# Kernel optimization log

Measured on AMD Instinct MI355X. Metric: run time of the kernel, lower is better.

The kernel has to match this reference:

```python
import jax, jax.numpy as jnp
import numpy as np

EPS = 1e-5


def _grid_edges(H, W):
    # radius_graph on the HxW integer grid with r=1.0, loop=False -> 4-neighbors,
    # then GCNConv's gcn_norm adds self-loops; we append them here once.
    idx = np.arange(H * W).reshape(H, W)
    r_s, r_d = idx[:, :-1].ravel(), idx[:, 1:].ravel()
    d_s, d_d = idx[:-1, :].ravel(), idx[1:, :].ravel()
    loop = np.arange(H * W)
    src = np.concatenate([r_s, r_d, d_s, d_d, loop])
    dst = np.concatenate([r_d, r_s, d_d, d_s, loop])
    return jnp.asarray(src, jnp.int32), jnp.asarray(dst, jnp.int32)


def _gcn_conv(x, W, b, src, dst, deg, dinv):
    # GCNConv(aggr='mean'): xw = x @ W; message = dinv[src]*dinv[dst] * xw[src];
    # mean-aggregate over incoming edges (incl. self-loop); add bias.
    xw = x @ W  # [B, N, Cout]
    w = (dinv[src] * dinv[dst])[None, :, None]
    agg = jnp.zeros((x.shape[0], x.shape[1], W.shape[1]), xw.dtype).at[:, dst].add(xw[:, src] * w)
    return agg / deg[None, :, None] + b


def _bn(x, gamma, beta):
    # BatchNorm2d, training-mode batch statistics (torch default), biased variance
    mu = x.mean(axis=(0, 2, 3), keepdims=True)
    var = ((x - mu) ** 2).mean(axis=(0, 2, 3), keepdims=True)
    return (x - mu) * jax.lax.rsqrt(var + EPS) * gamma[None, :, None, None] + beta[None, :, None, None]


def setup_inputs() -> dict:
    key = jax.random.key(0)
    ks = jax.random.split(key, 5)
    B, H, W, Cin, Cout = 8, 64, 64, 512, 512
    s = 0.02
    return {
        'x': jax.random.normal(ks[0], (B, H * W, Cin), jnp.float32),
        'H': H, 'W': W,
        'w_res': jax.random.normal(ks[1], (Cin, Cout), jnp.float32) * s,
        'w_pre': jax.random.normal(ks[2], (Cin, Cout), jnp.float32) * s,
        'b_pre': jnp.zeros((Cout,), jnp.float32),
        'w_g1': jax.random.normal(ks[3], (Cout, Cout), jnp.float32) * s,
        'b_g1': jnp.zeros((Cout,), jnp.float32),
        'w_g2': jax.random.normal(ks[4], (Cout, Cout), jnp.float32) * s,
        'b_g2': jnp.zeros((Cout,), jnp.float32),
        'g1': jnp.ones((Cout,), jnp.float32), 'beta1': jnp.zeros((Cout,), jnp.float32),
        'g2': jnp.ones((Cout,), jnp.float32), 'beta2': jnp.zeros((Cout,), jnp.float32),
    }


def reference(x, H, W, w_res, w_pre, b_pre, w_g1, b_g1, w_g2, b_g2, g1, beta1, g2, beta2):
    B, N, Cin = x.shape
    src, dst = _grid_edges(H, W)
    deg = jnp.zeros((N,), x.dtype).at[dst].add(1.0)  # in-degree incl. self-loops
    dinv = jax.lax.rsqrt(deg)
    # 1x1 convs on tokens == per-node matmuls
    residual = jnp.einsum('bnc,cd->bnd', x, w_res)
    xr = jnp.einsum('bnc,cd->bnd', x, w_pre) + b_pre
    h = jax.nn.relu(_gcn_conv(xr, w_g1, b_g1, src, dst, deg, dinv))
    h = jax.nn.relu(_gcn_conv(h, w_g2, b_g2, src, dst, deg, dinv))
    pooled = h.mean(axis=1)  # global_mean_pool -> [B, Cout]
    xg = _bn(pooled[:, :, None, None], g1, beta1)  # [B, Cout, 1, 1]
    res_img = residual.transpose(0, 2, 1).reshape(B, -1, H, W)
    return _bn(res_img + xg, g2, beta2)  # [B, Cout, H, W]
```

## Files before the change

kernel.cpp:

```cpp
#include <hip/hip_runtime.h>
#include <hip/hip_bf16.h>

using bf16 = __hip_bfloat16;
typedef __attribute__((ext_vector_type(8))) __bf16 bf16x8;
typedef __attribute__((ext_vector_type(4))) float f32x4;

__device__ __forceinline__ float bf2f(bf16 v) { return __bfloat162float(v); }
__device__ __forceinline__ bf16 f2bf(float f) { return __float2bfloat16(f); }

union bfu8 { bf16x8 v; bf16 h[8]; int4 i; };

__device__ __forceinline__ bool probeF32(const unsigned* probe) {
    return probe != nullptr && probe[0] == 0x3F800000u;
}
__device__ __forceinline__ float ldIn(const void* p, int i, bool f32) {
    return f32 ? ((const float*)p)[i] : bf2f(((const bf16*)p)[i]);
}

#define BATCH 8
#define GRID 64
#define NNODE 4096
#define CDIM 512
#define MROWS 32768
#define EPSBN 1e-5f

#define BM 128
#define BN 128
#define BK 32

__device__ __forceinline__ void gload16(bf16* lds, const bf16* g) {
    __builtin_amdgcn_global_load_lds(
        (const __attribute__((address_space(1))) unsigned int*)g,
        (__attribute__((address_space(3))) unsigned int*)lds, 16, 0, 0);
}

#define PIN() __builtin_amdgcn_sched_barrier(0)

__global__ __launch_bounds__(256) void gemm_lds(const bf16* __restrict__ A,
                                                const bf16* __restrict__ BT,
                                                bf16* __restrict__ C0,
                                                bf16* __restrict__ C1,
                                                const void* __restrict__ bias,
                                                const unsigned* __restrict__ probe,
                                                int K)
{
    __shared__ __align__(16) bf16 lA[2][BM * BK];
    __shared__ __align__(16) bf16 lB[2][BN * BK];

    const bool pf32 = probeF32(probe);
    const int tid  = threadIdx.x;
    const int bm = blockIdx.x, bn = blockIdx.y;
    const int wave = tid >> 6, lane = tid & 63;
    const int wr = (wave >> 1) * 64, wc = (wave & 1) * 64;
    const int lrow = lane & 15, quad = lane >> 4;

    f32x4 acc[4][4] = {};

    const bf16* Abase = A  + (size_t)bm * BM * K;
    const bf16* Bbase = BT + (size_t)bn * BN * K;

    const int srow = wave * 32 + (lane >> 2);
    const int scol = (lane & 3) * 8;
    const bf16* gA0 = Abase + (size_t)srow * K + scol;
    const bf16* gA1 = Abase + (size_t)(srow + 16) * K + scol;
    const bf16* gB0 = Bbase + (size_t)srow * K + scol;
    const bf16* gB1 = Bbase + (size_t)(srow + 16) * K + scol;
    bf16* laBase = &lA[0][0];
    bf16* lbBase = &lB[0][0];
    const int wofs = wave * 1024;

#define STAGE(BUF, TILE) do {                                              \
        const size_t koff_ = (size_t)(TILE) * BK;                          \
        gload16(laBase + (BUF) * (BM * BK) + wofs,       gA0 + koff_);     \
        gload16(laBase + (BUF) * (BM * BK) + wofs + 512, gA1 + koff_);     \
        gload16(lbBase + (BUF) * (BN * BK) + wofs,       gB0 + koff_);     \
        gload16(lbBase + (BUF) * (BN * BK) + wofs + 512, gB1 + koff_);     \
    } while (0)

#define COMPUTE(BUF) do {                                                  \
        const bf16* pA_ = laBase + (BUF) * (BM * BK);                      \
        const bf16* pB_ = lbBase + (BUF) * (BN * BK);                      \
        bf16x8 af[4], bv[4];                                               \
        _Pragma("unroll")                                                  \
        for (int i = 0; i < 4; ++i)                                        \
            af[i] = *(const bf16x8*)(pA_ + (wr + i * 16 + lrow) * BK + quad * 8); \
        _Pragma("unroll")                                                  \
        for (int j = 0; j < 4; ++j)                                        \
            bv[j] = *(const bf16x8*)(pB_ + (wc + j * 16 + lrow) * BK + quad * 8); \
        _Pragma("unroll")                                                  \
        for (int i = 0; i < 4; ++i)                                        \
            _Pragma("unroll")                                              \
            for (int j = 0; j < 4; ++j)                                    \
                acc[i][j] = __builtin_amdgcn_mfma_f32_16x16x32_bf16(af[i], bv[j], acc[i][j], 0, 0, 0); \
    } while (0)

    const int NT = K / BK;

    STAGE(0, 0);
    int t = 0;
    for (; t + 3 < NT; t += 2) {
        STAGE(1, t + 1);
        asm volatile("s_waitcnt vmcnt(4)" ::: "memory");
        __builtin_amdgcn_s_barrier(); PIN();
        COMPUTE(0);
        PIN(); __builtin_amdgcn_s_barrier(); PIN();

        STAGE(0, t + 2);
        asm volatile("s_waitcnt vmcnt(4)" ::: "memory");
        __builtin_amdgcn_s_barrier(); PIN();
        COMPUTE(1);
        PIN(); __builtin_amdgcn_s_barrier(); PIN();
    }
    STAGE(1, t + 1);
    asm volatile("s_waitcnt vmcnt(4)" ::: "memory");
    __builtin_amdgcn_s_barrier(); PIN();
    COMPUTE(0);
    PIN(); __builtin_amdgcn_s_barrier(); PIN();
    asm volatile("s_waitcnt vmcnt(0)" ::: "memory");
    __builtin_amdgcn_s_barrier(); PIN();
    COMPUTE(1);

#undef STAGE
#undef COMPUTE

    #pragma unroll
    for (int i = 0; i < 4; ++i) {
        const int mbase = bm * BM + wr + i * 16 + quad * 4;
        #pragma unroll
        for (int j = 0; j < 4; ++j) {
            int n = bn * BN + wc + j * 16 + lrow;
            bf16* Cd = C0;
            float bvv = 0.0f;
            if (C1 != nullptr && n >= CDIM) { Cd = C1; n -= CDIM; }
            else if (bias != nullptr)       { bvv = ldIn(bias, n, pf32); }
            #pragma unroll
            for (int rr = 0; rr < 4; ++rr)
                Cd[(size_t)(mbase + rr) * CDIM + n] = f2bf(acc[i][j][rr] + bvv);
        }
    }
}

__global__ __launch_bounds__(256) void convertX(const void* __restrict__ x,
                                                bf16* __restrict__ xb,
                                                const unsigned* __restrict__ probe)
{
    const bool f32 = probeF32(probe);
    const size_t i = ((size_t)blockIdx.x * 256 + threadIdx.x) * 8;
    if (f32) {
        const float4 u0 = *(const float4*)((const float*)x + i);
        const float4 u1 = *(const float4*)((const float*)x + i + 4);
        bf16 t[8] = { f2bf(u0.x), f2bf(u0.y), f2bf(u0.z), f2bf(u0.w),
                      f2bf(u1.x), f2bf(u1.y), f2bf(u1.z), f2bf(u1.w) };
        *(int4*)(xb + i) = *(const int4*)t;
    } else {
        *(int4*)(xb + i) = *(const int4*)((const bf16*)x + i);
    }
}

__global__ __launch_bounds__(256) void transpose512x4(const void* __restrict__ s0,
                                                      const void* __restrict__ s1,
                                                      const void* __restrict__ s2,
                                                      const void* __restrict__ s3,
                                                      bf16* __restrict__ dstBase,
                                                      const unsigned* __restrict__ probe)
{
    __shared__ float tile[64][65];
    const bool f32 = probeF32(probe);
    const int z = blockIdx.z;
    const void* src = (z == 0) ? s0 : (z == 1) ? s1 : (z == 2) ? s2 : s3;
    bf16* dst = dstBase + (size_t)z * 512 * 512;
    const int bx = blockIdx.x, by = blockIdx.y;
    const int t = threadIdx.x;
    const int col = t & 63, rbase = t >> 6;
    #pragma unroll 4
    for (int i = 0; i < 16; ++i) {
        int r = i * 4 + rbase;
        tile[r][col] = ldIn(src, (by * 64 + r) * 512 + bx * 64 + col, f32);
    }
    __syncthreads();
    #pragma unroll 4
    for (int i = 0; i < 16; ++i) {
        int r = i * 4 + rbase;
        dst[(size_t)(bx * 64 + r) * 512 + by * 64 + col] = f2bf(tile[col][r]);
    }
}

__device__ __forceinline__ float degOf(int y, int x) {
    return 1.0f + (y > 0) + (y < GRID - 1) + (x > 0) + (x < GRID - 1);
}

__global__ __launch_bounds__(256) void gcn_agg_v2(const bf16* __restrict__ T,
                                                  const void* __restrict__ bias,
                                                  const unsigned* __restrict__ probe,
                                                  bf16* __restrict__ H)
{
    const bool f32 = probeF32(probe);
    const int t = threadIdx.x;
    const int lane = t & 63, sub = t >> 6;
    const int n = blockIdx.x * 4 + sub;
    const int b = blockIdx.y;
    const int y = n >> 6, x = n & 63;
    const int cg = lane * 8;

    const float deg = degOf(y, x);
    const float dn  = rsqrtf(deg);
    const float inv = dn / deg;

    const bf16* cptr = T + ((size_t)b * NNODE + n) * CDIM + cg;

    bfu8 vc; vc.v = *(const bf16x8*)cptr;
    float s[8];
    #pragma unroll
    for (int j = 0; j < 8; ++j) s[j] = dn * bf2f(vc.h[j]);

    if (y > 0)        { float d = rsqrtf(degOf(y - 1, x)); bfu8 u; u.v = *(const bf16x8*)(cptr - 64 * CDIM);
                        #pragma unroll
                        for (int j = 0; j < 8; ++j) s[j] += d * bf2f(u.h[j]); }
    if (y < GRID - 1) { float d = rsqrtf(degOf(y + 1, x)); bfu8 u; u.v = *(const bf16x8*)(cptr + 64 * CDIM);
                        #pragma unroll
                        for (int j = 0; j < 8; ++j) s[j] += d * bf2f(u.h[j]); }
    if (x > 0)        { float d = rsqrtf(degOf(y, x - 1)); bfu8 u; u.v = *(const bf16x8*)(cptr - CDIM);
                        #pragma unroll
                        for (int j = 0; j < 8; ++j) s[j] += d * bf2f(u.h[j]); }
    if (x < GRID - 1) { float d = rsqrtf(degOf(y, x + 1)); bfu8 u; u.v = *(const bf16x8*)(cptr + CDIM);
                        #pragma unroll
                        for (int j = 0; j < 8; ++j) s[j] += d * bf2f(u.h[j]); }

    bfu8 o;
    #pragma unroll
    for (int j = 0; j < 8; ++j)
        o.h[j] = f2bf(fmaxf(s[j] * inv + ldIn(bias, cg + j, f32), 0.0f));
    *(int4*)(H + ((size_t)b * NNODE + n) * CDIM + cg) = o.i;
}

__global__ __launch_bounds__(256) void gcn_agg_pool_v3(const bf16* __restrict__ T,
                                                       const void* __restrict__ bias,
                                                       const unsigned* __restrict__ probe,
                                                       float* __restrict__ poolPart)
{
    const bool f32 = probeF32(probe);
    const int y = blockIdx.x;
    const int b = blockIdx.y;
    const int t = threadIdx.x;
    const int lane = t & 63, sub = t >> 6;
    const int cg = lane * 8;

    const bf16* base = T + (size_t)b * NNODE * CDIM;

    float biasv[8];
    #pragma unroll
    for (int j = 0; j < 8; ++j) biasv[j] = ldIn(bias, cg + j, f32);

    float acc[8] = {};

    for (int xi = 0; xi < 16; ++xi) {
        const int x = sub * 16 + xi;
        const int n = y * 64 + x;
        const float deg = degOf(y, x);
        const float dn  = rsqrtf(deg);
        const float inv = dn / deg;
        const bf16* cptr = base + (size_t)n * CDIM + cg;

        bfu8 vc; vc.v = *(const bf16x8*)cptr;
        float s[8];
        #pragma unroll
        for (int j = 0; j < 8; ++j) s[j] = dn * bf2f(vc.h[j]);

        if (y > 0)        { float d = rsqrtf(degOf(y - 1, x)); bfu8 u; u.v = *(const bf16x8*)(cptr - 64 * CDIM);
                            #pragma unroll
                            for (int j = 0; j < 8; ++j) s[j] += d * bf2f(u.h[j]); }
        if (y < GRID - 1) { float d = rsqrtf(degOf(y + 1, x)); bfu8 u; u.v = *(const bf16x8*)(cptr + 64 * CDIM);
                            #pragma unroll
                            for (int j = 0; j < 8; ++j) s[j] += d * bf2f(u.h[j]); }
        if (x > 0)        { float d = rsqrtf(degOf(y, x - 1)); bfu8 u; u.v = *(const bf16x8*)(cptr - CDIM);
                            #pragma unroll
                            for (int j = 0; j < 8; ++j) s[j] += d * bf2f(u.h[j]); }
        if (x < GRID - 1) { float d = rsqrtf(degOf(y, x + 1)); bfu8 u; u.v = *(const bf16x8*)(cptr + CDIM);
                            #pragma unroll
                            for (int j = 0; j < 8; ++j) s[j] += d * bf2f(u.h[j]); }

        #pragma unroll
        for (int j = 0; j < 8; ++j)
            acc[j] += fmaxf(s[j] * inv + biasv[j], 0.0f);
    }

    __shared__ float red[4][64][9];
    #pragma unroll
    for (int j = 0; j < 8; ++j) red[sub][lane][j] = acc[j];
    __syncthreads();
    if (sub == 0) {
        float* dst = poolPart + (size_t)(b * GRID + y) * CDIM + cg;
        #pragma unroll
        for (int j = 0; j < 8; ++j)
            dst[j] = red[0][lane][j] + red[1][lane][j] + red[2][lane][j] + red[3][lane][j];
    }
}

__global__ void bn1_kernel(const float* __restrict__ poolPart,
                           const void* __restrict__ g1, const void* __restrict__ beta1,
                           const unsigned* __restrict__ probe,
                           float* __restrict__ xg)
{
    const bool f32 = probeF32(probe);
    const int c = blockIdx.x * 256 + threadIdx.x;
    float p[BATCH];
    float mu = 0.0f;
    #pragma unroll
    for (int b = 0; b < BATCH; ++b) {
        float a0 = 0, a1 = 0, a2 = 0, a3 = 0;
        const float* src = poolPart + (size_t)b * GRID * CDIM + c;
        #pragma unroll 4
        for (int y = 0; y < GRID; y += 4) {
            a0 += src[(size_t)(y + 0) * CDIM];
            a1 += src[(size_t)(y + 1) * CDIM];
            a2 += src[(size_t)(y + 2) * CDIM];
            a3 += src[(size_t)(y + 3) * CDIM];
        }
        p[b] = (a0 + a1 + a2 + a3) * (1.0f / (float)NNODE);
        mu += p[b];
    }
    mu *= (1.0f / (float)BATCH);
    float var = 0.0f;
    #pragma unroll
    for (int b = 0; b < BATCH; ++b) { float d = p[b] - mu; var += d * d; }
    var *= (1.0f / (float)BATCH);
    const float rs = rsqrtf(var + EPSBN) * ldIn(g1, c, f32);
    const float bt = ldIn(beta1, c, f32);
    #pragma unroll
    for (int b = 0; b < BATCH; ++b)
        xg[b * CDIM + c] = (p[b] - mu) * rs + bt;
}

__global__ __launch_bounds__(256) void bn2_stats_part(const bf16* __restrict__ R,
                                                      const float* __restrict__ xg,
                                                      float* __restrict__ bn2Part)
{
    const int t = threadIdx.x;
    const int lane = t & 63, sub = t >> 6;
    const int cg = lane * 8;
    const int row0 = blockIdx.x * 128;
    const int b = row0 >> 12;

    float xgv[8];
    #pragma unroll
    for (int j = 0; j < 8; ++j) xgv[j] = xg[b * CDIM + cg + j];

    float s[8] = {}, q[8] = {};
    #pragma unroll
    for (int i0 = 0; i0 < 4; ++i0) {
        const bf16* base = R + (size_t)(row0 + i0 * 32 + sub * 8) * CDIM + cg;
        #pragma unroll
        for (int k = 0; k < 8; ++k) {
            bfu8 u; u.v = *(const bf16x8*)(base + (size_t)k * CDIM);
            #pragma unroll
            for (int j = 0; j < 8; ++j) {
                float v = bf2f(u.h[j]) + xgv[j];
                s[j] += v; q[j] += v * v;
            }
        }
    }

    __shared__ float redS[4][64][9], redQ[4][64][9];
    #pragma unroll
    for (int j = 0; j < 8; ++j) { redS[sub][lane][j] = s[j]; redQ[sub][lane][j] = q[j]; }
    __syncthreads();
    if (sub == 0) {
        float* dst = bn2Part + (size_t)blockIdx.x * 1024;
        #pragma unroll
        for (int j = 0; j < 8; ++j) {
            dst[cg + j]       = redS[0][lane][j] + redS[1][lane][j] + redS[2][lane][j] + redS[3][lane][j];
            dst[512 + cg + j] = redQ[0][lane][j] + redQ[1][lane][j] + redQ[2][lane][j] + redQ[3][lane][j];
        }
    }
}

__global__ void bn2_reduce(const float* __restrict__ bn2Part, float* __restrict__ sums)
{
    const int c = blockIdx.x * 256 + threadIdx.x;
    float a0 = 0, a1 = 0, a2 = 0, a3 = 0, a4 = 0, a5 = 0, a6 = 0, a7 = 0;
    #pragma unroll 4
    for (int blk = 0; blk < 256; blk += 8) {
        a0 += bn2Part[(size_t)(blk + 0) * 1024 + c];
        a1 += bn2Part[(size_t)(blk + 1) * 1024 + c];
        a2 += bn2Part[(size_t)(blk + 2) * 1024 + c];
        a3 += bn2Part[(size_t)(blk + 3) * 1024 + c];
        a4 += bn2Part[(size_t)(blk + 4) * 1024 + c];
        a5 += bn2Part[(size_t)(blk + 5) * 1024 + c];
        a6 += bn2Part[(size_t)(blk + 6) * 1024 + c];
        a7 += bn2Part[(size_t)(blk + 7) * 1024 + c];
    }
    sums[c] = ((a0 + a1) + (a2 + a3)) + ((a4 + a5) + (a6 + a7));
}

__global__ void bn2_final(const float* __restrict__ sums, const float* __restrict__ xg,
                          const void* __restrict__ g2, const void* __restrict__ beta2,
                          const unsigned* __restrict__ probe,
                          float* __restrict__ scale, float* __restrict__ tshift)
{
    const bool f32 = probeF32(probe);
    const int c = blockIdx.x * 256 + threadIdx.x;
    const float mu  = sums[c] * (1.0f / (float)MROWS);
    const float var = sums[512 + c] * (1.0f / (float)MROWS) - mu * mu;
    const float sc  = ldIn(g2, c, f32) * rsqrtf(var + EPSBN);
    scale[c] = sc;
    const float base = ldIn(beta2, c, f32) - mu * sc;
    #pragma unroll
    for (int b = 0; b < BATCH; ++b)
        tshift[b * CDIM + c] = xg[b * CDIM + c] * sc + base;
}

__global__ __launch_bounds__(256) void out_transpose(const bf16* __restrict__ R,
                                                     const float* __restrict__ scale,
                                                     const float* __restrict__ tshift,
                                                     const unsigned* __restrict__ probe,
                                                     void* __restrict__ outv)
{
    __shared__ float tile[64][65];
    const bool f32 = probeF32(probe);
    const int nt = blockIdx.x;
    const int ct = blockIdx.y;
    const int b  = blockIdx.z;
    const int t = threadIdx.x;
    const int c0 = ct * 64, n0 = nt * 64;

    const int rr  = t >> 3;
    const int cch = (t & 7) * 8;
    #pragma unroll
    for (int half = 0; half < 2; ++half) {
        int r = rr + half * 32;
        bfu8 u; u.v = *(const bf16x8*)(R + ((size_t)(b * NNODE + n0 + r)) * CDIM + c0 + cch);
        #pragma unroll
        for (int j = 0; j < 8; ++j) tile[r][cch + j] = bf2f(u.h[j]);
    }
    __syncthreads();

    const int col = t & 63, rbase = t >> 6;
    if (f32) {
        float* out = (float*)outv;
        #pragma unroll 4
        for (int i = 0; i < 16; ++i) {
            int cc = i * 4 + rbase;
            float sc  = scale[c0 + cc];
            float tsh = tshift[b * CDIM + c0 + cc];
            out[((size_t)(b * CDIM + c0 + cc)) * NNODE + n0 + col] = tile[col][cc] * sc + tsh;
        }
    } else {
        bf16* out = (bf16*)outv;
        #pragma unroll 4
        for (int i = 0; i < 16; ++i) {
            int cc = i * 4 + rbase;
            float sc  = scale[c0 + cc];
            float tsh = tshift[b * CDIM + c0 + cc];
            out[((size_t)(b * CDIM + c0 + cc)) * NNODE + n0 + col] = f2bf(tile[col][cc] * sc + tsh);
        }
    }
}

extern "C" void kernel_launch(void* const* d_in, const int* in_sizes, int n_in,
                              void* d_out, int out_size, void* d_ws, size_t ws_size,
                              hipStream_t stream)
{
    const void* x     = d_in[0];
    const void* w_res = d_in[3];
    const void* w_pre = d_in[4];
    const void* b_pre = d_in[5];
    const void* w_g1  = d_in[6];
    const void* b_g1  = d_in[7];
    const void* w_g2  = d_in[8];
    const void* b_g2  = d_in[9];
    const void* g1    = d_in[10];
    const void* beta1 = d_in[11];
    const void* g2    = d_in[12];
    const void* beta2 = d_in[13];
    const unsigned* probe = (const unsigned*)g1;

    char* ws = (char*)d_ws;
    constexpr size_t WSZ = (size_t)512 * 512 * 2;

    bf16* BTpre = (bf16*)(ws);
    bf16* BTg1  = (bf16*)(ws + 2 * WSZ);
    bf16* BTg2  = (bf16*)(ws + 3 * WSZ);
    char* smallb = ws + 4 * WSZ;
    float* sums   = (float*)(smallb);
    float* xg     = (float*)(smallb + 4096);
    float* scale  = (float*)(smallb + 4096 + 16384);
    float* tshift = (float*)(smallb + 4096 + 16384 + 2048);
    bf16* Rres = (bf16*)(smallb + 65536);

    char* dA = (char*)d_out;
    char* dB = (char*)d_out + (size_t)MROWS * CDIM * 2;

    bf16* XR = (bf16*)dA;
    bf16* Tt = (bf16*)dB;
    float* poolPart = (float*)dA;
    float* bn2Part  = (float*)(dA + (1 << 20));

    transpose512x4<<<dim3(8, 8, 4), 256, 0, stream>>>(w_pre, w_res, w_g1, w_g2,
                                                      BTpre, probe);

    dim3 blk(256);
    convertX<<<dim3(MROWS * CDIM / (256 * 8)), blk, 0, stream>>>(x, Tt, probe);
    gemm_lds<<<dim3(MROWS / BM, 1024 / BN), blk, 0, stream>>>(Tt, BTpre, XR, Rres, b_pre, probe, CDIM);
    gemm_lds<<<dim3(MROWS / BM, CDIM / BN), blk, 0, stream>>>(XR, BTg1, Tt, nullptr, nullptr, nullptr, CDIM);
    gcn_agg_v2<<<dim3(NNODE / 4, BATCH), blk, 0, stream>>>(Tt, b_g1, probe, XR);
    gemm_lds<<<dim3(MROWS / BM, CDIM / BN), blk, 0, stream>>>(XR, BTg2, Tt, nullptr, nullptr, nullptr, CDIM);
    gcn_agg_pool_v3<<<dim3(GRID, BATCH), blk, 0, stream>>>(Tt, b_g2, probe, poolPart);
    bn1_kernel<<<dim3(2), blk, 0, stream>>>(poolPart, g1, beta1, probe, xg);
    bn2_stats_part<<<dim3(MROWS / 128), blk, 0, stream>>>(Rres, xg, bn2Part);
    bn2_reduce<<<dim3(4), blk, 0, stream>>>(bn2Part, sums);
    bn2_final<<<dim3(2), blk, 0, stream>>>(sums, xg, g2, beta2, probe, scale, tshift);
    out_transpose<<<dim3(NNODE / 64, CDIM / 64, BATCH), blk, 0, stream>>>(Rres, scale, tshift, probe, d_out);
}
```

Measured before the change: 397.8 us.

## Fold pre-projection weight into first GCN weight to drop a large GEMM

Precomputes the combined weight W_pre·W_g1 with a small 512x512 GEMM, along with the matching bias vector b_pre·W_g1, so the first big GEMM produces both the residual and the first GCN projection directly from x. This removes the full 32768x512x512 GEMM that previously turned the pre-projection output into the GCN input, plus its intermediate write and read. The cost is an extra small GEMM and a bias kernel, and the folded weight is rounded once more to bf16 before use.

```diff
diff --git a/kernel.cpp b/kernel.cpp
--- a/kernel.cpp
+++ b/kernel.cpp
@@ -40,14 +40,12 @@
                                                 const bf16* __restrict__ BT,
                                                 bf16* __restrict__ C0,
                                                 bf16* __restrict__ C1,
-                                                const void* __restrict__ bias,
-                                                const unsigned* __restrict__ probe,
+                                                const float* __restrict__ bias,
                                                 int K)
 {
     __shared__ __align__(16) bf16 lA[2][BM * BK];
     __shared__ __align__(16) bf16 lB[2][BN * BK];
 
-    const bool pf32 = probeF32(probe);
     const int tid  = threadIdx.x;
     const int bm = blockIdx.x, bn = blockIdx.y;
     const int wave = tid >> 6, lane = tid & 63;
@@ -132,7 +130,7 @@
             bf16* Cd = C0;
             float bvv = 0.0f;
             if (C1 != nullptr && n >= CDIM) { Cd = C1; n -= CDIM; }
-            else if (bias != nullptr)       { bvv = ldIn(bias, n, pf32); }
+            else if (bias != nullptr)       { bvv = bias[n]; }
             #pragma unroll
             for (int rr = 0; rr < 4; ++rr)
                 Cd[(size_t)(mbase + rr) * CDIM + n] = f2bf(acc[i][j][rr] + bvv);
@@ -157,21 +155,31 @@
     }
 }
 
-__global__ __launch_bounds__(256) void transpose512x4(const void* __restrict__ s0,
-                                                      const void* __restrict__ s1,
-                                                      const void* __restrict__ s2,
-                                                      const void* __restrict__ s3,
-                                                      bf16* __restrict__ dstBase,
-                                                      const unsigned* __restrict__ probe)
+__global__ __launch_bounds__(256) void weightPrep(const void* __restrict__ s0,
+                                                  const void* __restrict__ s1,
+                                                  const void* __restrict__ s2,
+                                                  const void* __restrict__ s3,
+                                                  bf16* __restrict__ dstBase,
+                                                  const unsigned* __restrict__ probe)
 {
     __shared__ float tile[64][65];
     const bool f32 = probeF32(probe);
     const int z = blockIdx.z;
     const void* src = (z == 0) ? s0 : (z == 1) ? s1 : (z == 2) ? s2 : s3;
-    bf16* dst = dstBase + (size_t)z * 512 * 512;
+    bf16* dst = dstBase + (size_t)(z + 1) * 512 * 512;
     const int bx = blockIdx.x, by = blockIdx.y;
     const int t = threadIdx.x;
     const int col = t & 63, rbase = t >> 6;
+
+    if (z == 3) {
+        #pragma unroll 4
+        for (int i = 0; i < 16; ++i) {
+            int r = i * 4 + rbase;
+            size_t idx = (size_t)(by * 64 + r) * 512 + bx * 64 + col;
+            dst[idx] = f2bf(ldIn(src, idx, f32));
+        }
+        return;
+    }
     #pragma unroll 4
     for (int i = 0; i < 16; ++i) {
         int r = i * 4 + rbase;
@@ -183,6 +191,23 @@
         int r = i * 4 + rbase;
         dst[(size_t)(bx * 64 + r) * 512 + by * 64 + col] = f2bf(tile[col][r]);
     }
+}
+
+__global__ void bc1_kernel(const void* __restrict__ b_pre,
+                           const bf16* __restrict__ BTg1,
+                           const unsigned* __restrict__ probe,
+                           float* __restrict__ bc1)
+{
+    const bool f32 = probeF32(probe);
+    const int e = blockIdx.x * 256 + threadIdx.x;
+    float s = 0.0f;
+    for (int d0 = 0; d0 < 512; d0 += 8) {
+        bfu8 u; u.v = *(const bf16x8*)(BTg1 + (size_t)e * 512 + d0);
+        #pragma unroll
+        for (int j = 0; j < 8; ++j)
+            s += ldIn(b_pre, d0 + j, f32) * bf2f(u.h[j]);
+    }
+    bc1[e] = s;
 }
 
 __device__ __forceinline__ float degOf(int y, int x) {
@@ -477,34 +502,39 @@
     char* ws = (char*)d_ws;
     constexpr size_t WSZ = (size_t)512 * 512 * 2;
 
-    bf16* BTpre = (bf16*)(ws);
+    bf16* BTc1  = (bf16*)(ws);
+    bf16* BTres = (bf16*)(ws + WSZ);
     bf16* BTg1  = (bf16*)(ws + 2 * WSZ);
     bf16* BTg2  = (bf16*)(ws + 3 * WSZ);
-    char* smallb = ws + 4 * WSZ;
+    bf16* Wpre_b= (bf16*)(ws + 4 * WSZ);
+    char* smallb = ws + 5 * WSZ;
     float* sums   = (float*)(smallb);
     float* xg     = (float*)(smallb + 4096);
     float* scale  = (float*)(smallb + 4096 + 16384);
     float* tshift = (float*)(smallb + 4096 + 16384 + 2048);
+    float* bc1    = (float*)(smallb + 4096 + 16384 + 2048 + 16384);
     bf16* Rres = (bf16*)(smallb + 65536);
 
     char* dA = (char*)d_out;
     char* dB = (char*)d_out + (size_t)MROWS * CDIM * 2;
 
-    bf16* XR = (bf16*)dA;
-    bf16* Tt = (bf16*)dB;
-    float* poolPart = (float*)dA;
-    float* bn2Part  = (float*)(dA + (1 << 20));
-
-    transpose512x4<<<dim3(8, 8, 4), 256, 0, stream>>>(w_pre, w_res, w_g1, w_g2,
-                                                      BTpre, probe);
+    bf16* Ta = (bf16*)dA;
+    bf16* Xb = (bf16*)dB;
+    float* poolPart = (float*)dB;
+    float* bn2Part  = (float*)(dB + (1 << 20));
 
     dim3 blk(256);
-    convertX<<<dim3(MROWS * CDIM / (256 * 8)), blk, 0, stream>>>(x, Tt, probe);
-    gemm_lds<<<dim3(MROWS / BM, 1024 / BN), blk, 0, stream>>>(Tt, BTpre, XR, Rres, b_pre, probe, CDIM);
-    gemm_lds<<<dim3(MROWS / BM, CDIM / BN), blk, 0, stream>>>(XR, BTg1, Tt, nullptr, nullptr, nullptr, CDIM);
-    gcn_agg_v2<<<dim3(NNODE / 4, BATCH), blk, 0, stream>>>(Tt, b_g1, probe, XR);
-    gemm_lds<<<dim3(MROWS / BM, CDIM / BN), blk, 0, stream>>>(XR, BTg2, Tt, nullptr, nullptr, nullptr, CDIM);
-    gcn_agg_pool_v3<<<dim3(GRID, BATCH), blk, 0, stream>>>(Tt, b_g2, probe, poolPart);
+
+    weightPrep<<<dim3(8, 8, 4), blk, 0, stream>>>(w_res, w_g1, w_g2, w_pre,
+                                                  (bf16*)ws, probe);
+    convertX<<<dim3(MROWS * CDIM / (256 * 8)), blk, 0, stream>>>(x, Xb, probe);
+    gemm_lds<<<dim3(512 / BM, 512 / BN), blk, 0, stream>>>(BTg1, Wpre_b, BTc1,
+                                                           nullptr, nullptr, CDIM);
+    bc1_kernel<<<dim3(2), blk, 0, stream>>>(b_pre, BTg1, probe, bc1);
+    gemm_lds<<<dim3(MROWS / BM, 1024 / BN), blk, 0, stream>>>(Xb, BTc1, Ta, Rres, bc1, CDIM);
+    gcn_agg_v2<<<dim3(NNODE / 4, BATCH), blk, 0, stream>>>(Ta, b_g1, probe, Xb);
+    gemm_lds<<<dim3(MROWS / BM, CDIM / BN), blk, 0, stream>>>(Xb, BTg2, Ta, nullptr, nullptr, CDIM);
+    gcn_agg_pool_v3<<<dim3(GRID, BATCH), blk, 0, stream>>>(Ta, b_g2, probe, poolPart);
     bn1_kernel<<<dim3(2), blk, 0, stream>>>(poolPart, g1, beta1, probe, xg);
     bn2_stats_part<<<dim3(MROWS / 128), blk, 0, stream>>>(Rres, xg, bn2Part);
     bn2_reduce<<<dim3(4), blk, 0, stream>>>(bn2Part, sums);
```

Measured after the change: 406.4 us. 1.02x slower.

## Decouple BN2 stats from xg algebraically and vectorize GEMM epilogue stores

Applied to the files above, without the earlier changes.

BN2 statistics of the residual are now computed right after the first GEMM, without the pooled xg term. The xg contribution is added back analytically per batch in one merged bn_all kernel, which replaces the bn1, bn2_reduce and bn2_final launches. The GEMM swaps MFMA operand order so each lane holds 4 consecutive columns, which allows 8-byte vector stores in the epilogue. This adds an extra workspace buffer for the partials, and the E[x^2]-mu^2 variance form may lose some precision.

```diff
diff --git a/kernel.cpp b/kernel.cpp
--- a/kernel.cpp
+++ b/kernel.cpp
@@ -9,6 +9,7 @@
 __device__ __forceinline__ bf16 f2bf(float f) { return __float2bfloat16(f); }
 
 union bfu8 { bf16x8 v; bf16 h[8]; int4 i; };
+union bfu4 { bf16 h[4]; uint2 u; };
 
 __device__ __forceinline__ bool probeF32(const unsigned* probe) {
     return probe != nullptr && probe[0] == 0x3F800000u;
@@ -91,7 +92,7 @@
         for (int i = 0; i < 4; ++i)                                        \
             _Pragma("unroll")                                              \
             for (int j = 0; j < 4; ++j)                                    \
-                acc[i][j] = __builtin_amdgcn_mfma_f32_16x16x32_bf16(af[i], bv[j], acc[i][j], 0, 0, 0); \
+                acc[i][j] = __builtin_amdgcn_mfma_f32_16x16x32_bf16(bv[j], af[i], acc[i][j], 0, 0, 0); \
     } while (0)
 
     const int NT = K / BK;
@@ -123,19 +124,24 @@
 #undef STAGE
 #undef COMPUTE
 
+    const bool toC1 = (C1 != nullptr) && (bn >= CDIM / BN);
+    bf16* Cd = toC1 ? C1 : C0;
+    const bool addB = (!toC1) && (bias != nullptr);
+    const int nbase = (toC1 ? (bn - CDIM / BN) : bn) * BN + wc + quad * 4;
+    const int mrow0 = bm * BM + wr + lrow;
     #pragma unroll
     for (int i = 0; i < 4; ++i) {
-        const int mbase = bm * BM + wr + i * 16 + quad * 4;
+        const int m = mrow0 + i * 16;
         #pragma unroll
         for (int j = 0; j < 4; ++j) {
-            int n = bn * BN + wc + j * 16 + lrow;
-            bf16* Cd = C0;
-            float bvv = 0.0f;
-            if (C1 != nullptr && n >= CDIM) { Cd = C1; n -= CDIM; }
-            else if (bias != nullptr)       { bvv = ldIn(bias, n, pf32); }
+            const int n0 = nbase + j * 16;
+            bfu4 o;
             #pragma unroll
-            for (int rr = 0; rr < 4; ++rr)
-                Cd[(size_t)(mbase + rr) * CDIM + n] = f2bf(acc[i][j][rr] + bvv);
+            for (int rr = 0; rr < 4; ++rr) {
+                float bvv = addB ? ldIn(bias, n0 + rr, pf32) : 0.0f;
+                o.h[rr] = f2bf(acc[i][j][rr] + bvv);
+            }
+            *(uint2*)(Cd + (size_t)m * CDIM + n0) = o.u;
         }
     }
 }
@@ -296,15 +302,55 @@
     }
 }
 
-__global__ void bn1_kernel(const float* __restrict__ poolPart,
-                           const void* __restrict__ g1, const void* __restrict__ beta1,
-                           const unsigned* __restrict__ probe,
-                           float* __restrict__ xg)
+__global__ __launch_bounds__(256) void bn2_stats_part(const bf16* __restrict__ R,
+                                                      float* __restrict__ bn2Part)
+{
+    const int t = threadIdx.x;
+    const int lane = t & 63, sub = t >> 6;
+    const int cg = lane * 8;
+    const int row0 = blockIdx.x * 128;
+
+    float s[8] = {}, q[8] = {};
+    #pragma unroll
+    for (int i0 = 0; i0 < 4; ++i0) {
+        const bf16* base = R + (size_t)(row0 + i0 * 32 + sub * 8) * CDIM + cg;
+        #pragma unroll
+        for (int k = 0; k < 8; ++k) {
+            bfu8 u; u.v = *(const bf16x8*)(base + (size_t)k * CDIM);
+            #pragma unroll
+            for (int j = 0; j < 8; ++j) {
+                float v = bf2f(u.h[j]);
+                s[j] += v; q[j] += v * v;
+            }
+        }
+    }
+
+    __shared__ float redS[4][64][9], redQ[4][64][9];
+    #pragma unroll
+    for (int j = 0; j < 8; ++j) { redS[sub][lane][j] = s[j]; redQ[sub][lane][j] = q[j]; }
+    __syncthreads();
+    if (sub == 0) {
+        float* dst = bn2Part + (size_t)blockIdx.x * 1024;
+        #pragma unroll
+        for (int j = 0; j < 8; ++j) {
+            dst[cg + j]       = redS[0][lane][j] + redS[1][lane][j] + redS[2][lane][j] + redS[3][lane][j];
+            dst[512 + cg + j] = redQ[0][lane][j] + redQ[1][lane][j] + redQ[2][lane][j] + redQ[3][lane][j];
+        }
+    }
+}
+
+__global__ void bn_all(const float* __restrict__ poolPart,
+                       const float* __restrict__ bn2Part,
+                       const void* __restrict__ g1, const void* __restrict__ beta1,
+                       const void* __restrict__ g2, const void* __restrict__ beta2,
+                       const unsigned* __restrict__ probe,
+                       float* __restrict__ scale, float* __restrict__ tshift)
 {
     const bool f32 = probeF32(probe);
     const int c = blockIdx.x * 256 + threadIdx.x;
+
     float p[BATCH];
-    float mu = 0.0f;
+    float mu1 = 0.0f;
     #pragma unroll
     for (int b = 0; b < BATCH; ++b) {
         float a0 = 0, a1 = 0, a2 = 0, a3 = 0;
@@ -317,96 +363,40 @@
             a3 += src[(size_t)(y + 3) * CDIM];
         }
         p[b] = (a0 + a1 + a2 + a3) * (1.0f / (float)NNODE);
-        mu += p[b];
-    }
-    mu *= (1.0f / (float)BATCH);
-    float var = 0.0f;
-    #pragma unroll
-    for (int b = 0; b < BATCH; ++b) { float d = p[b] - mu; var += d * d; }
-    var *= (1.0f / (float)BATCH);
-    const float rs = rsqrtf(var + EPSBN) * ldIn(g1, c, f32);
-    const float bt = ldIn(beta1, c, f32);
-    #pragma unroll
-    for (int b = 0; b < BATCH; ++b)
-        xg[b * CDIM + c] = (p[b] - mu) * rs + bt;
-}
-
-__global__ __launch_bounds__(256) void bn2_stats_part(const bf16* __restrict__ R,
-                                                      const float* __restrict__ xg,
-                                                      float* __restrict__ bn2Part)
-{
-    const int t = threadIdx.x;
-    const int lane = t & 63, sub = t >> 6;
-    const int cg = lane * 8;
-    const int row0 = blockIdx.x * 128;
-    const int b = row0 >> 12;
-
-    float xgv[8];
-    #pragma unroll
-    for (int j = 0; j < 8; ++j) xgv[j] = xg[b * CDIM + cg + j];
-
-    float s[8] = {}, q[8] = {};
-    #pragma unroll
-    for (int i0 = 0; i0 < 4; ++i0) {
-        const bf16* base = R + (size_t)(row0 + i0 * 32 + sub * 8) * CDIM + cg;
-        #pragma unroll
-        for (int k = 0; k < 8; ++k) {
-            bfu8 u; u.v = *(const bf16x8*)(base + (size_t)k * CDIM);
-            #pragma unroll
-            for (int j = 0; j < 8; ++j) {
-                float v = bf2f(u.h[j]) + xgv[j];
-                s[j] += v; q[j] += v * v;
-            }
-        }
-    }
-
-    __shared__ float redS[4][64][9], redQ[4][64][9];
-    #pragma unroll
-    for (int j = 0; j < 8; ++j) { redS[sub][lane][j] = s[j]; redQ[sub][lane][j] = q[j]; }
-    __syncthreads();
-    if (sub == 0) {
-        float* dst = bn2Part + (size_t)blockIdx.x * 1024;
-        #pragma unroll
-        for (int j = 0; j < 8; ++j) {
-            dst[cg + j]       = redS[0][lane][j] + redS[1][lane][j] + redS[2][lane][j] + redS[3][lane][j];
-            dst[512 + cg + j] = redQ[0][lane][j] + redQ[1][lane][j] + redQ[2][lane][j] + redQ[3][lane][j];
-        }
-    }
-}
-
-__global__ void bn2_reduce(const float* __restrict__ bn2Part, float* __restrict__ sums)
-{
-    const int c = blockIdx.x * 256 + threadIdx.x;
-    float a0 = 0, a1 = 0, a2 = 0, a3 = 0, a4 = 0, a5 = 0, a6 = 0, a7 = 0;
-    #pragma unroll 4
-    for (int blk = 0; blk < 256; blk += 8) {
-        a0 += bn2Part[(size_t)(blk + 0) * 1024 + c];
-        a1 += bn2Part[(size_t)(blk + 1) * 1024 + c];
-        a2 += bn2Part[(size_t)(blk + 2) * 1024 + c];
-        a3 += bn2Part[(size_t)(blk + 3) * 1024 + c];
-        a4 += bn2Part[(size_t)(blk + 4) * 1024 + c];
-        a5 += bn2Part[(size_t)(blk + 5) * 1024 + c];
-        a6 += bn2Part[(size_t)(blk + 6) * 1024 + c];
-        a7 += bn2Part[(size_t)(blk + 7) * 1024 + c];
-    }
-    sums[c] = ((a0 + a1) + (a2 + a3)) + ((a4 + a5) + (a6 + a7));
-}
-
-__global__ void bn2_final(const float* __restrict__ sums, const float* __restrict__ xg,
-                          const void* __restrict__ g2, const void* __restrict__ beta2,
-                          const unsigned* __restrict__ probe,
-                          float* __restrict__ scale, float* __restrict__ tshift)
-{
-    const bool f32 = probeF32(probe);
-    const int c = blockIdx.x * 256 + threadIdx.x;
-    const float mu  = sums[c] * (1.0f / (float)MROWS);
-    const float var = sums[512 + c] * (1.0f / (float)MROWS) - mu * mu;
+        mu1 += p[b];
+    }
+    mu1 *= (1.0f / (float)BATCH);
+    float var1 = 0.0f;
+    #pragma unroll
+    for (int b = 0; b < BATCH; ++b) { float d = p[b] - mu1; var1 += d * d; }
+    var1 *= (1.0f / (float)BATCH);
+    const float rs1 = rsqrtf(var1 + EPSBN) * ldIn(g1, c, f32);
+    const float bt1 = ldIn(beta1, c, f32);
+    float xg[BATCH];
+    #pragma unroll
+    for (int b = 0; b < BATCH; ++b) xg[b] = (p[b] - mu1) * rs1 + bt1;
+
+    float sAll = 0.0f, qAll = 0.0f;
+    #pragma unroll
+    for (int b = 0; b < BATCH; ++b) {
+        float S = 0.0f, Q = 0.0f;
+        const float* src = bn2Part + (size_t)b * 32 * 1024 + c;
+        #pragma unroll 4
+        for (int blk = 0; blk < 32; ++blk) {
+            S += src[(size_t)blk * 1024];
+            Q += src[(size_t)blk * 1024 + 512];
+        }
+        sAll += S + (float)NNODE * xg[b];
+        qAll += Q + 2.0f * xg[b] * S + (float)NNODE * xg[b] * xg[b];
+    }
+    const float mu  = sAll * (1.0f / (float)MROWS);
+    const float var = qAll * (1.0f / (float)MROWS) - mu * mu;
     const float sc  = ldIn(g2, c, f32) * rsqrtf(var + EPSBN);
     scale[c] = sc;
     const float base = ldIn(beta2, c, f32) - mu * sc;
     #pragma unroll
     for (int b = 0; b < BATCH; ++b)
-        tshift[b * CDIM + c] = xg[b * CDIM + c] * sc + base;
+        tshift[b * CDIM + c] = xg[b] * sc + base;
 }
 
 __global__ __launch_bounds__(256) void out_transpose(const bf16* __restrict__ R,
@@ -481,11 +471,10 @@
     bf16* BTg1  = (bf16*)(ws + 2 * WSZ);
     bf16* BTg2  = (bf16*)(ws + 3 * WSZ);
     char* smallb = ws + 4 * WSZ;
-    float* sums   = (float*)(smallb);
-    float* xg     = (float*)(smallb + 4096);
-    float* scale  = (float*)(smallb + 4096 + 16384);
-    float* tshift = (float*)(smallb + 4096 + 16384 + 2048);
+    float* scale  = (float*)(smallb);
+    float* tshift = (float*)(smallb + 2048);
     bf16* Rres = (bf16*)(smallb + 65536);
+    float* bn2Part = (float*)(smallb + 65536 + (size_t)MROWS * CDIM * 2);
 
     char* dA = (char*)d_out;
     char* dB = (char*)d_out + (size_t)MROWS * CDIM * 2;
@@ -493,21 +482,19 @@
     bf16* XR = (bf16*)dA;
     bf16* Tt = (bf16*)dB;
     float* poolPart = (float*)dA;
-    float* bn2Part  = (float*)(dA + (1 << 20));
-
-    transpose512x4<<<dim3(8, 8, 4), 256, 0, stream>>>(w_pre, w_res, w_g1, w_g2,
+
+    dim3 blk(256);
+
+    transpose512x4<<<dim3(8, 8, 4), blk, 0, stream>>>(w_pre, w_res, w_g1, w_g2,
                                                       BTpre, probe);
-
-    dim3 blk(256);
     convertX<<<dim3(MROWS * CDIM / (256 * 8)), blk, 0, stream>>>(x, Tt, probe);
     gemm_lds<<<dim3(MROWS / BM, 1024 / BN), blk, 0, stream>>>(Tt, BTpre, XR, Rres, b_pre, probe, CDIM);
+    bn2_stats_part<<<dim3(MROWS / 128), blk, 0, stream>>>(Rres, bn2Part);
     gemm_lds<<<dim3(MROWS / BM, CDIM / BN), blk, 0, stream>>>(XR, BTg1, Tt, nullptr, nullptr, nullptr, CDIM);
     gcn_agg_v2<<<dim3(NNODE / 4, BATCH), blk, 0, stream>>>(Tt, b_g1, probe, XR);
     gemm_lds<<<dim3(MROWS / BM, CDIM / BN), blk, 0, stream>>>(XR, BTg2, Tt, nullptr, nullptr, nullptr, CDIM);
     gcn_agg_pool_v3<<<dim3(GRID, BATCH), blk, 0, stream>>>(Tt, b_g2, probe, poolPart);
-    bn1_kernel<<<dim3(2), blk, 0, stream>>>(poolPart, g1, beta1, probe, xg);
-    bn2_stats_part<<<dim3(MROWS / 128), blk, 0, stream>>>(Rres, xg, bn2Part);
-    bn2_reduce<<<dim3(4), blk, 0, stream>>>(bn2Part, sums);
-    bn2_final<<<dim3(2), blk, 0, stream>>>(sums, xg, g2, beta2, probe, scale, tshift);
+    bn_all<<<dim3(2), blk, 0, stream>>>(poolPart, bn2Part, g1, beta1, g2, beta2,
+                                        probe, scale, tshift);
     out_transpose<<<dim3(NNODE / 64, CDIM / 64, BATCH), blk, 0, stream>>>(Rres, scale, tshift, probe, d_out);
 }
```

Measured after the change: 410.5 us. +3.2%, slower.
